# Kernel tuning notes

Measured on AMD Instinct MI355X. Metric: run time of the kernel, lower is better.

## Reference

```python
import jax, jax.numpy as jnp
import numpy as np

N = 100_000
E = 1_600_000
IN_FT, HID, OUT = 512, 128, 64


def setup_inputs() -> dict:
    key = jax.random.key(0)
    ks = jax.random.split(key, 7)
    x = jax.random.normal(ks[0], (N, IN_FT), dtype=jnp.float32)
    edge_index = jax.random.randint(ks[1], (2, E), 0, N, dtype=jnp.int32)
    edge_weight = jax.random.uniform(ks[2], (E,), dtype=jnp.float32)
    W1 = jax.random.normal(ks[3], (IN_FT, HID), dtype=jnp.float32) * 0.05
    b1 = jnp.zeros((HID,), dtype=jnp.float32)
    W2 = jax.random.normal(ks[4], (HID, OUT), dtype=jnp.float32) * 0.05
    b2 = jnp.zeros((OUT,), dtype=jnp.float32)
    return {"x": x, "edge_index": edge_index, "edge_weight": edge_weight,
            "W1": W1, "b1": b1, "W2": W2, "b2": b2}


def reference(x, edge_index, edge_weight, W1, b1, W2, b2):
    n = x.shape[0]
    row, col = edge_index[0], edge_index[1]
    # PyG gcn_norm: add self-loops with weight 1, symmetric normalization
    loop = jnp.arange(n, dtype=row.dtype)
    r = jnp.concatenate([row, loop])
    c = jnp.concatenate([col, loop])
    w = jnp.concatenate([edge_weight, jnp.ones((n,), edge_weight.dtype)])
    deg = jax.ops.segment_sum(w, c, num_segments=n)
    dinv = jnp.where(deg > 0, jax.lax.rsqrt(deg), 0.0)
    norm = dinv[r] * w * dinv[c]  # [E + N]

    def conv(h, W, b):
        h = h @ W                                  # [N, F_out]
        msg = norm[:, None] * h[r]                 # gather source nodes
        return jax.ops.segment_sum(msg, c, num_segments=n) + b

    h = jax.nn.relu(conv(x, W1, b1))
    # dropout: inference mode (training=False) -> identity
    out = conv(h, W2, b2)
    return jax.nn.log_softmax(out, axis=1)
```

## Files before the change

kernel.cpp:

```cpp
#include <hip/hip_runtime.h>
#include <hip/hip_fp16.h>


constexpr int NN  = 100000;
constexpr int NE  = 1600000;
constexpr int FIN = 512;
constexpr int FH  = 128;
constexpr int FO  = 64;
constexpr int CAP = 64;

constexpr int NBLK1 = 512;
constexpr int EPB   = NE / NBLK1;
constexpr int NBKT  = 196;
constexpr int BCAP  = 9728;

constexpr float WSCALE  = 32767.0f;
constexpr float IWSCALE = 1.0f / 32767.0f;

typedef _Float16 f16x8 __attribute__((ext_vector_type(8)));
typedef float    f32x4 __attribute__((ext_vector_type(4)));

union F16Frag { short4 s[2]; f16x8 v; };


__global__ __launch_bounds__(256) void k_prep(const float* __restrict__ W1,
                                              const float* __restrict__ W2,
                                              int* __restrict__ bcur,
                                              _Float16* __restrict__ w1t,
                                              _Float16* __restrict__ w2t) {
    int i = blockIdx.x * 256 + threadIdx.x;
    if (i < NBKT) bcur[i] = 0;
    if (i < FIN * FH) {
        int k = i >> 7, c = i & 127;
        w1t[c * FIN + k] = (_Float16)W1[i];
    } else if (i < FIN * FH + FH * FO) {
        int j = i - FIN * FH;
        int k = j >> 6, c = j & 63;
        w2t[c * FH + k] = (_Float16)W2[j];
    }
}


__global__ __launch_bounds__(256) void k_pass1(const int* __restrict__ rowi,
                                               const int* __restrict__ coli,
                                               const float* __restrict__ ew,
                                               int* __restrict__ bcur,
                                               unsigned long long* __restrict__ binned) {
    __shared__ unsigned long long buf[EPB];
    __shared__ int hist[NBKT];
    __shared__ int curs[NBKT];
    const int t = threadIdx.x;
    const int base = blockIdx.x * EPB;
    for (int i = t; i < NBKT; i += 256) hist[i] = 0;
    __syncthreads();
    for (int i = t; i < EPB; i += 256) {
        int e = base + i;
        int c = coli[e];
        unsigned wq = __float2uint_rn(ew[e] * WSCALE);
        buf[i] = ((unsigned long long)(unsigned)c << 32)
               | (unsigned long long)((wq << 17) | (unsigned)rowi[e]);
        atomicAdd(&hist[c >> 9], 1);
    }
    __syncthreads();
    if (t < NBKT) curs[t] = atomicAdd(&bcur[t], hist[t]);
    __syncthreads();
    for (int i = t; i < EPB; i += 256) {
        unsigned long long v = buf[i];
        int b = (int)(v >> 41);
        int pos = atomicAdd(&curs[b], 1);
        if ((unsigned)pos < BCAP) binned[(size_t)b * BCAP + pos] = v;
    }
}


__global__ __launch_bounds__(256) void k_pass2(const int* __restrict__ bcur,
                                               const unsigned long long* __restrict__ binned,
                                               unsigned* __restrict__ pay,
                                               int* __restrict__ cursor,
                                               float* __restrict__ dinv) {
    __shared__ int   cnt[512];
    __shared__ float wsum[512];
    const int t = threadIdx.x, b = blockIdx.x;
    for (int i = t; i < 512; i += 256) { cnt[i] = 0; wsum[i] = 0.f; }
    __syncthreads();
    const int total = min(bcur[b], BCAP);
    const int nbase = b * 512;
    for (int i = t; i < total; i += 256) {
        unsigned long long v = binned[(size_t)b * BCAP + i];
        int c9 = (int)((v >> 32) & 511);
        unsigned lo = (unsigned)v;
        int pos = atomicAdd(&cnt[c9], 1);
        atomicAdd(&wsum[c9], (float)(lo >> 17) * IWSCALE);
        if (pos < CAP) pay[(size_t)(nbase + c9) * CAP + pos] = lo;
    }
    __syncthreads();
    for (int i = t; i < 512; i += 256) {
        int node = nbase + i;
        if (node < NN) {
            cursor[node] = cnt[i];
            dinv[node]   = rsqrtf(1.0f + wsum[i]);
        }
    }
}


__global__ __launch_bounds__(256) void k_gemm1(const float* __restrict__ X,
                                               const _Float16* __restrict__ w1t,
                                               _Float16* __restrict__ H1) {
    __shared__ __align__(16) _Float16 As[128 * 64];
    __shared__ __align__(16) _Float16 Bs[128 * 64];
    const int tid  = threadIdx.x;
    const int brow = blockIdx.x * 128;
    const int wid = tid >> 6, l = tid & 63;
    const int wr = wid >> 1, wc = wid & 1;
    const int l15 = l & 15, lg = l >> 4;

    f32x4 acc[4][4];
#pragma unroll
    for (int m = 0; m < 4; ++m)
#pragma unroll
        for (int n = 0; n < 4; ++n) acc[m][n] = (f32x4){0.f, 0.f, 0.f, 0.f};

    const int ar  = tid >> 1;
    const int as0 = (tid & 1) * 4;
    const int grow = brow + ar;

    for (int k0 = 0; k0 < FIN; k0 += 64) {
#pragma unroll
        for (int i = 0; i < 4; ++i) {
            int slot = as0 + i;
            float4 lo = make_float4(0.f, 0.f, 0.f, 0.f), hi = lo;
            if (grow < NN) {
                lo = *(const float4*)&X[(size_t)grow * FIN + k0 + slot * 8];
                hi = *(const float4*)&X[(size_t)grow * FIN + k0 + slot * 8 + 4];
            }
            union { _Float16 h[8]; int4 v; } pk;
            pk.h[0] = (_Float16)lo.x; pk.h[1] = (_Float16)lo.y;
            pk.h[2] = (_Float16)lo.z; pk.h[3] = (_Float16)lo.w;
            pk.h[4] = (_Float16)hi.x; pk.h[5] = (_Float16)hi.y;
            pk.h[6] = (_Float16)hi.z; pk.h[7] = (_Float16)hi.w;
            *(int4*)&As[ar * 64 + ((slot ^ (ar & 7)) * 8)] = pk.v;
        }
#pragma unroll
        for (int i = 0; i < 4; ++i) {
            int slot = as0 + i;
            *(int4*)&Bs[ar * 64 + ((slot ^ (ar & 7)) * 8)] =
                *(const int4*)&w1t[ar * FIN + k0 + slot * 8];
        }
        __syncthreads();
#pragma unroll
        for (int ks = 0; ks < 2; ++ks) {
            F16Frag au[4], bu[4];
            int klo = ks * 32 + 4 * lg;
            int khi = klo + 16;
#pragma unroll
            for (int m = 0; m < 4; ++m) {
                int row = wr * 64 + m * 16 + l15;
                int sw  = row & 7;
                au[m].s[0] = *(const short4*)&As[row * 64 + (((klo >> 3) ^ sw) * 8) + (klo & 7)];
                au[m].s[1] = *(const short4*)&As[row * 64 + (((khi >> 3) ^ sw) * 8) + (khi & 7)];
            }
#pragma unroll
            for (int n = 0; n < 4; ++n) {
                int row = wc * 64 + n * 16 + l15;
                int sw  = row & 7;
                bu[n].s[0] = *(const short4*)&Bs[row * 64 + (((klo >> 3) ^ sw) * 8) + (klo & 7)];
                bu[n].s[1] = *(const short4*)&Bs[row * 64 + (((khi >> 3) ^ sw) * 8) + (khi & 7)];
            }
#pragma unroll
            for (int m = 0; m < 4; ++m)
#pragma unroll
                for (int n = 0; n < 4; ++n)
                    acc[m][n] = __builtin_amdgcn_mfma_f32_16x16x32_f16(
                        au[m].v, bu[n].v, acc[m][n], 0, 0, 0);
        }
        __syncthreads();
    }
#pragma unroll
    for (int m = 0; m < 4; ++m)
#pragma unroll
        for (int n = 0; n < 4; ++n) {
            int gcol = wc * 64 + n * 16 + l15;
#pragma unroll
            for (int r = 0; r < 4; ++r) {
                int gr = brow + wr * 64 + m * 16 + lg * 4 + r;
                if (gr < NN) H1[(size_t)gr * FH + gcol] = (_Float16)acc[m][n][r];
            }
        }
}


__global__ __launch_bounds__(256) void k_gemm2(const _Float16* __restrict__ H2,
                                               const _Float16* __restrict__ w2t,
                                               _Float16* __restrict__ H3) {
    __shared__ __align__(16) _Float16 As[128 * 128];
    __shared__ __align__(16) _Float16 Bs[64 * 128];
    const int tid  = threadIdx.x;
    const int brow = blockIdx.x * 128;
    const int wid = tid >> 6, l = tid & 63;
    const int wr = wid >> 1, wc = wid & 1;
    const int l15 = l & 15, lg = l >> 4;

    f32x4 acc[4][2];
#pragma unroll
    for (int m = 0; m < 4; ++m)
#pragma unroll
        for (int n = 0; n < 2; ++n) acc[m][n] = (f32x4){0.f, 0.f, 0.f, 0.f};

    {
        int ar = tid >> 1, grow = brow + ar;
#pragma unroll
        for (int i = 0; i < 8; ++i) {
            int slot = (tid & 1) * 8 + i;
            int4 v = make_int4(0, 0, 0, 0);
            if (grow < NN) v = *(const int4*)&H2[(size_t)grow * FH + slot * 8];
            *(int4*)&As[ar * 128 + ((slot ^ (ar & 15)) * 8)] = v;
        }
        int br = tid >> 2;
#pragma unroll
        for (int i = 0; i < 4; ++i) {
            int slot = (tid & 3) * 4 + i;
            *(int4*)&Bs[br * 128 + ((slot ^ (br & 15)) * 8)] =
                *(const int4*)&w2t[br * FH + slot * 8];
        }
    }
    __syncthreads();
#pragma unroll
    for (int ks = 0; ks < 4; ++ks) {
        F16Frag au[4], bu[2];
        int klo = ks * 32 + 4 * lg;
        int khi = klo + 16;
#pragma unroll
        for (int m = 0; m < 4; ++m) {
            int row = wr * 64 + m * 16 + l15;
            int sw  = row & 15;
            au[m].s[0] = *(const short4*)&As[row * 128 + (((klo >> 3) ^ sw) * 8) + (klo & 7)];
            au[m].s[1] = *(const short4*)&As[row * 128 + (((khi >> 3) ^ sw) * 8) + (khi & 7)];
        }
#pragma unroll
        for (int n = 0; n < 2; ++n) {
            int row = wc * 32 + n * 16 + l15;
            int sw  = row & 15;
            bu[n].s[0] = *(const short4*)&Bs[row * 128 + (((klo >> 3) ^ sw) * 8) + (klo & 7)];
            bu[n].s[1] = *(const short4*)&Bs[row * 128 + (((khi >> 3) ^ sw) * 8) + (khi & 7)];
        }
#pragma unroll
        for (int m = 0; m < 4; ++m)
#pragma unroll
            for (int n = 0; n < 2; ++n)
                acc[m][n] = __builtin_amdgcn_mfma_f32_16x16x32_f16(
                    au[m].v, bu[n].v, acc[m][n], 0, 0, 0);
    }
#pragma unroll
    for (int m = 0; m < 4; ++m)
#pragma unroll
        for (int n = 0; n < 2; ++n) {
            int gcol = wc * 32 + n * 16 + l15;
#pragma unroll
            for (int r = 0; r < 4; ++r) {
                int gr = brow + wr * 64 + m * 16 + lg * 4 + r;
                if (gr < NN) H3[(size_t)gr * FO + gcol] = (_Float16)acc[m][n][r];
            }
        }
}


__global__ __launch_bounds__(256) void k_agg1(const int* __restrict__ cursor,
                                              const unsigned* __restrict__ pay,
                                              const float* __restrict__ dinv,
                                              const __half* __restrict__ H1,
                                              const float* __restrict__ b1,
                                              __half* __restrict__ H2) {
    int node = (blockIdx.x * 256 + threadIdx.x) >> 6;
    int lane = threadIdx.x & 63;
    if (node >= NN) return;
    const int f = lane * 2;
    float dc = dinv[node];
    float2 hc = __half22float2(*(const __half2*)&H1[(size_t)node * FH + f]);
    float a0x = dc * dc * hc.x, a0y = dc * dc * hc.y;
    float a1x = 0, a1y = 0, a2x = 0, a2y = 0, a3x = 0, a3y = 0;
    int cnt = min(max(cursor[node], 0), CAP);
    const unsigned* p = &pay[(size_t)node * CAP];
    int e = 0;
    for (; e + 4 <= cnt; e += 4) {
        unsigned v0 = p[e], v1 = p[e + 1], v2 = p[e + 2], v3 = p[e + 3];
        int s0 = v0 & 0x1FFFF, s1 = v1 & 0x1FFFF;
        int s2 = v2 & 0x1FFFF, s3 = v3 & 0x1FFFF;
        float w0 = (float)(v0 >> 17) * IWSCALE * dinv[s0] * dc;
        float w1 = (float)(v1 >> 17) * IWSCALE * dinv[s1] * dc;
        float w2 = (float)(v2 >> 17) * IWSCALE * dinv[s2] * dc;
        float w3 = (float)(v3 >> 17) * IWSCALE * dinv[s3] * dc;
        float2 g0 = __half22float2(*(const __half2*)&H1[(size_t)s0 * FH + f]);
        float2 g1 = __half22float2(*(const __half2*)&H1[(size_t)s1 * FH + f]);
        float2 g2 = __half22float2(*(const __half2*)&H1[(size_t)s2 * FH + f]);
        float2 g3 = __half22float2(*(const __half2*)&H1[(size_t)s3 * FH + f]);
        a0x += w0 * g0.x; a0y += w0 * g0.y;
        a1x += w1 * g1.x; a1y += w1 * g1.y;
        a2x += w2 * g2.x; a2y += w2 * g2.y;
        a3x += w3 * g3.x; a3y += w3 * g3.y;
    }
    for (; e < cnt; ++e) {
        unsigned v = p[e];
        int s = v & 0x1FFFF;
        float w = (float)(v >> 17) * IWSCALE * dinv[s] * dc;
        float2 g = __half22float2(*(const __half2*)&H1[(size_t)s * FH + f]);
        a0x += w * g.x; a0y += w * g.y;
    }
    float vx = a0x + a1x + a2x + a3x + b1[f];
    float vy = a0y + a1y + a2y + a3y + b1[f + 1];
    vx = vx > 0.f ? vx : 0.f;
    vy = vy > 0.f ? vy : 0.f;
    *(__half2*)&H2[(size_t)node * FH + f] = __floats2half2_rn(vx, vy);
}


__global__ __launch_bounds__(256) void k_agg2(const int* __restrict__ cursor,
                                              const unsigned* __restrict__ pay,
                                              const float* __restrict__ dinv,
                                              const __half* __restrict__ H3,
                                              const float* __restrict__ b2,
                                              float* __restrict__ out) {
    int node = (blockIdx.x * 256 + threadIdx.x) >> 6;
    int lane = threadIdx.x & 63;
    if (node >= NN) return;
    float dc = dinv[node];
    float a0 = dc * dc * __half2float(H3[(size_t)node * FO + lane]);
    float a1 = 0, a2 = 0, a3 = 0;
    int cnt = min(max(cursor[node], 0), CAP);
    const unsigned* p = &pay[(size_t)node * CAP];
    int e = 0;
    for (; e + 4 <= cnt; e += 4) {
        unsigned v0 = p[e], v1 = p[e + 1], v2 = p[e + 2], v3 = p[e + 3];
        int s0 = v0 & 0x1FFFF, s1 = v1 & 0x1FFFF;
        int s2 = v2 & 0x1FFFF, s3 = v3 & 0x1FFFF;
        float w0 = (float)(v0 >> 17) * IWSCALE * dinv[s0] * dc;
        float w1 = (float)(v1 >> 17) * IWSCALE * dinv[s1] * dc;
        float w2 = (float)(v2 >> 17) * IWSCALE * dinv[s2] * dc;
        float w3 = (float)(v3 >> 17) * IWSCALE * dinv[s3] * dc;
        a0 += w0 * __half2float(H3[(size_t)s0 * FO + lane]);
        a1 += w1 * __half2float(H3[(size_t)s1 * FO + lane]);
        a2 += w2 * __half2float(H3[(size_t)s2 * FO + lane]);
        a3 += w3 * __half2float(H3[(size_t)s3 * FO + lane]);
    }
    for (; e < cnt; ++e) {
        unsigned v = p[e];
        int s = v & 0x1FFFF;
        float w = (float)(v >> 17) * IWSCALE * dinv[s] * dc;
        a0 += w * __half2float(H3[(size_t)s * FO + lane]);
    }
    float v = a0 + a1 + a2 + a3 + b2[lane];
    float m = v;
#pragma unroll
    for (int s = 32; s; s >>= 1) m = fmaxf(m, __shfl_xor(m, s));
    float ex = expf(v - m);
    float sum = ex;
#pragma unroll
    for (int s = 32; s; s >>= 1) sum += __shfl_xor(sum, s);
    out[(size_t)node * FO + lane] = v - m - logf(sum);
}


extern "C" void kernel_launch(void* const* d_in, const int* in_sizes, int n_in,
                              void* d_out, int out_size, void* d_ws, size_t ws_size,
                              hipStream_t stream) {
    const float* x   = (const float*)d_in[0];
    const int*   ei  = (const int*)d_in[1];
    const int*   row = ei;
    const int*   col = ei + NE;
    const float* ew  = (const float*)d_in[2];
    const float* W1  = (const float*)d_in[3];
    const float* b1  = (const float*)d_in[4];
    const float* W2  = (const float*)d_in[5];
    const float* b2  = (const float*)d_in[6];
    float* out = (float*)d_out;

    int*       bcur   = (int*)d_ws;
    int*       cursor = bcur + 256;
    float*     dinv   = (float*)(cursor + 102400);
    _Float16*  w1t    = (_Float16*)(dinv + 102400);
    _Float16*  w2t    = w1t + FIN * FH;
    unsigned long long* binned = (unsigned long long*)(w2t + FH * FO);
    unsigned*  pay    = (unsigned*)(binned + (size_t)NBKT * BCAP);
    _Float16*  H1     = (_Float16*)(pay + (size_t)NN * CAP);
    _Float16*  H2     = H1 + (size_t)NN * FH;
    _Float16*  H3     = H2 + (size_t)NN * FH;

    k_prep <<<(FIN * FH + FH * FO + 255) / 256, 256, 0, stream>>>(W1, W2, bcur, w1t, w2t);
    k_pass1<<<NBLK1, 256, 0, stream>>>(row, col, ew, bcur, binned);
    k_pass2<<<NBKT, 256, 0, stream>>>(bcur, binned, pay, cursor, dinv);

    k_gemm1<<<(NN + 127) / 128, 256, 0, stream>>>(x, w1t, H1);
    k_agg1 <<<(NN * 64 + 255) / 256, 256, 0, stream>>>(cursor, pay, dinv,
                                                       (const __half*)H1, b1, (__half*)H2);
    k_gemm2<<<(NN + 127) / 128, 256, 0, stream>>>(H2, w2t, H3);
    k_agg2 <<<(NN * 64 + 255) / 256, 256, 0, stream>>>(cursor, pay, dinv,
                                                       (const __half*)H3, b2, out);
}
```

Measured before the change: 287.4 us.

## Halve GEMM row tiles and register-prefetch next K-slice in gemm1

Both GEMM kernels now use 64-row tiles instead of 128, which doubles the grid size and raises occupancy through launch_bounds(256,4). In gemm1, the next 64-wide K slice of X and W1 is loaded into registers while the current slice is staged into shared memory and multiplied, so global-load latency overlaps with MFMA work. The aim is to hide the cost of streaming X, the 200MB fp32 input that dominates. The trade-off is more blocks that each reload the W tile, and less MFMA reuse per block.

```diff
diff --git a/kernel.cpp b/kernel.cpp
--- a/kernel.cpp
+++ b/kernel.cpp
@@ -104,58 +104,74 @@
 }
 
 
-__global__ __launch_bounds__(256) void k_gemm1(const float* __restrict__ X,
-                                               const _Float16* __restrict__ w1t,
-                                               _Float16* __restrict__ H1) {
-    __shared__ __align__(16) _Float16 As[128 * 64];
+__global__ __launch_bounds__(256, 4) void k_gemm1(const float* __restrict__ X,
+                                                  const _Float16* __restrict__ w1t,
+                                                  _Float16* __restrict__ H1) {
+    __shared__ __align__(16) _Float16 As[64 * 64];
     __shared__ __align__(16) _Float16 Bs[128 * 64];
     const int tid  = threadIdx.x;
-    const int brow = blockIdx.x * 128;
+    const int brow = blockIdx.x * 64;
     const int wid = tid >> 6, l = tid & 63;
     const int wr = wid >> 1, wc = wid & 1;
     const int l15 = l & 15, lg = l >> 4;
 
-    f32x4 acc[4][4];
-#pragma unroll
-    for (int m = 0; m < 4; ++m)
+    f32x4 acc[2][4];
+#pragma unroll
+    for (int m = 0; m < 2; ++m)
 #pragma unroll
         for (int n = 0; n < 4; ++n) acc[m][n] = (f32x4){0.f, 0.f, 0.f, 0.f};
 
-    const int ar  = tid >> 1;
-    const int as0 = (tid & 1) * 4;
+    const int ar   = tid >> 2;
+    const int apart= tid & 3;
     const int grow = brow + ar;
+    const int br   = tid >> 1;
+    const int bhalf= tid & 1;
+
+    float4 xa[4];
+    int4   wb[4];
+
+#pragma unroll
+    for (int j = 0; j < 4; ++j) {
+        xa[j] = (grow < NN) ? *(const float4*)&X[(size_t)grow * FIN + apart * 16 + j * 4]
+                            : make_float4(0.f, 0.f, 0.f, 0.f);
+        wb[j] = *(const int4*)&w1t[br * FIN + bhalf * 32 + j * 8];
+    }
 
     for (int k0 = 0; k0 < FIN; k0 += 64) {
 #pragma unroll
-        for (int i = 0; i < 4; ++i) {
-            int slot = as0 + i;
-            float4 lo = make_float4(0.f, 0.f, 0.f, 0.f), hi = lo;
-            if (grow < NN) {
-                lo = *(const float4*)&X[(size_t)grow * FIN + k0 + slot * 8];
-                hi = *(const float4*)&X[(size_t)grow * FIN + k0 + slot * 8 + 4];
+        for (int h = 0; h < 2; ++h) {
+            union { _Float16 f[8]; int4 v; } pk;
+            float4 a = xa[h * 2], b = xa[h * 2 + 1];
+            pk.f[0] = (_Float16)a.x; pk.f[1] = (_Float16)a.y;
+            pk.f[2] = (_Float16)a.z; pk.f[3] = (_Float16)a.w;
+            pk.f[4] = (_Float16)b.x; pk.f[5] = (_Float16)b.y;
+            pk.f[6] = (_Float16)b.z; pk.f[7] = (_Float16)b.w;
+            int slot = apart * 2 + h;
+            *(int4*)&As[ar * 64 + ((slot ^ (ar & 7)) * 8)] = pk.v;
+        }
+#pragma unroll
+        for (int j = 0; j < 4; ++j) {
+            int slot = bhalf * 4 + j;
+            *(int4*)&Bs[br * 64 + ((slot ^ (br & 7)) * 8)] = wb[j];
+        }
+        if (k0 + 64 < FIN) {
+#pragma unroll
+            for (int j = 0; j < 4; ++j) {
+                xa[j] = (grow < NN)
+                    ? *(const float4*)&X[(size_t)grow * FIN + k0 + 64 + apart * 16 + j * 4]
+                    : make_float4(0.f, 0.f, 0.f, 0.f);
+                wb[j] = *(const int4*)&w1t[br * FIN + k0 + 64 + bhalf * 32 + j * 8];
             }
-            union { _Float16 h[8]; int4 v; } pk;
-            pk.h[0] = (_Float16)lo.x; pk.h[1] = (_Float16)lo.y;
-            pk.h[2] = (_Float16)lo.z; pk.h[3] = (_Float16)lo.w;
-            pk.h[4] = (_Float16)hi.x; pk.h[5] = (_Float16)hi.y;
-            pk.h[6] = (_Float16)hi.z; pk.h[7] = (_Float16)hi.w;
-            *(int4*)&As[ar * 64 + ((slot ^ (ar & 7)) * 8)] = pk.v;
-        }
-#pragma unroll
-        for (int i = 0; i < 4; ++i) {
-            int slot = as0 + i;
-            *(int4*)&Bs[ar * 64 + ((slot ^ (ar & 7)) * 8)] =
-                *(const int4*)&w1t[ar * FIN + k0 + slot * 8];
         }
         __syncthreads();
 #pragma unroll
         for (int ks = 0; ks < 2; ++ks) {
-            F16Frag au[4], bu[4];
+            F16Frag au[2], bu[4];
             int klo = ks * 32 + 4 * lg;
             int khi = klo + 16;
 #pragma unroll
-            for (int m = 0; m < 4; ++m) {
-                int row = wr * 64 + m * 16 + l15;
+            for (int m = 0; m < 2; ++m) {
+                int row = wr * 32 + m * 16 + l15;
                 int sw  = row & 7;
                 au[m].s[0] = *(const short4*)&As[row * 64 + (((klo >> 3) ^ sw) * 8) + (klo & 7)];
                 au[m].s[1] = *(const short4*)&As[row * 64 + (((khi >> 3) ^ sw) * 8) + (khi & 7)];
@@ -168,7 +184,7 @@
                 bu[n].s[1] = *(const short4*)&Bs[row * 64 + (((khi >> 3) ^ sw) * 8) + (khi & 7)];
             }
 #pragma unroll
-            for (int m = 0; m < 4; ++m)
+            for (int m = 0; m < 2; ++m)
 #pragma unroll
                 for (int n = 0; n < 4; ++n)
                     acc[m][n] = __builtin_amdgcn_mfma_f32_16x16x32_f16(
@@ -177,62 +193,57 @@
         __syncthreads();
     }
 #pragma unroll
-    for (int m = 0; m < 4; ++m)
+    for (int m = 0; m < 2; ++m)
 #pragma unroll
         for (int n = 0; n < 4; ++n) {
             int gcol = wc * 64 + n * 16 + l15;
 #pragma unroll
             for (int r = 0; r < 4; ++r) {
-                int gr = brow + wr * 64 + m * 16 + lg * 4 + r;
+                int gr = brow + wr * 32 + m * 16 + lg * 4 + r;
                 if (gr < NN) H1[(size_t)gr * FH + gcol] = (_Float16)acc[m][n][r];
             }
         }
 }
 
 
-__global__ __launch_bounds__(256) void k_gemm2(const _Float16* __restrict__ H2,
-                                               const _Float16* __restrict__ w2t,
-                                               _Float16* __restrict__ H3) {
-    __shared__ __align__(16) _Float16 As[128 * 128];
+__global__ __launch_bounds__(256, 4) void k_gemm2(const _Float16* __restrict__ H2,
+                                                  const _Float16* __restrict__ w2t,
+                                                  _Float16* __restrict__ H3) {
+    __shared__ __align__(16) _Float16 As[64 * 128];
     __shared__ __align__(16) _Float16 Bs[64 * 128];
     const int tid  = threadIdx.x;
-    const int brow = blockIdx.x * 128;
+    const int brow = blockIdx.x * 64;
     const int wid = tid >> 6, l = tid & 63;
     const int wr = wid >> 1, wc = wid & 1;
     const int l15 = l & 15, lg = l >> 4;
 
-    f32x4 acc[4][2];
-#pragma unroll
-    for (int m = 0; m < 4; ++m)
+    f32x4 acc[2][2];
+#pragma unroll
+    for (int m = 0; m < 2; ++m)
 #pragma unroll
         for (int n = 0; n < 2; ++n) acc[m][n] = (f32x4){0.f, 0.f, 0.f, 0.f};
 
     {
-        int ar = tid >> 1, grow = brow + ar;
-#pragma unroll
-        for (int i = 0; i < 8; ++i) {
-            int slot = (tid & 1) * 8 + i;
+        int ar = tid >> 2, part = tid & 3, grow = brow + ar;
+#pragma unroll
+        for (int j = 0; j < 4; ++j) {
+            int slot = part * 4 + j;
             int4 v = make_int4(0, 0, 0, 0);
             if (grow < NN) v = *(const int4*)&H2[(size_t)grow * FH + slot * 8];
             *(int4*)&As[ar * 128 + ((slot ^ (ar & 15)) * 8)] = v;
-        }
-        int br = tid >> 2;
-#pragma unroll
-        for (int i = 0; i < 4; ++i) {
-            int slot = (tid & 3) * 4 + i;
-            *(int4*)&Bs[br * 128 + ((slot ^ (br & 15)) * 8)] =
-                *(const int4*)&w2t[br * FH + slot * 8];
+            *(int4*)&Bs[ar * 128 + ((slot ^ (ar & 15)) * 8)] =
+                *(const int4*)&w2t[ar * FH + slot * 8];
         }
     }
     __syncthreads();
 #pragma unroll
     for (int ks = 0; ks < 4; ++ks) {
-        F16Frag au[4], bu[2];
+        F16Frag au[2], bu[2];
         int klo = ks * 32 + 4 * lg;
         int khi = klo + 16;
 #pragma unroll
-        for (int m = 0; m < 4; ++m) {
-            int row = wr * 64 + m * 16 + l15;
+        for (int m = 0; m < 2; ++m) {
+            int row = wr * 32 + m * 16 + l15;
             int sw  = row & 15;
             au[m].s[0] = *(const short4*)&As[row * 128 + (((klo >> 3) ^ sw) * 8) + (klo & 7)];
             au[m].s[1] = *(const short4*)&As[row * 128 + (((khi >> 3) ^ sw) * 8) + (khi & 7)];
@@ -245,20 +256,20 @@
             bu[n].s[1] = *(const short4*)&Bs[row * 128 + (((khi >> 3) ^ sw) * 8) + (khi & 7)];
         }
 #pragma unroll
-        for (int m = 0; m < 4; ++m)
+        for (int m = 0; m < 2; ++m)
 #pragma unroll
             for (int n = 0; n < 2; ++n)
                 acc[m][n] = __builtin_amdgcn_mfma_f32_16x16x32_f16(
                     au[m].v, bu[n].v, acc[m][n], 0, 0, 0);
     }
 #pragma unroll
-    for (int m = 0; m < 4; ++m)
+    for (int m = 0; m < 2; ++m)
 #pragma unroll
         for (int n = 0; n < 2; ++n) {
             int gcol = wc * 32 + n * 16 + l15;
 #pragma unroll
             for (int r = 0; r < 4; ++r) {
-                int gr = brow + wr * 64 + m * 16 + lg * 4 + r;
+                int gr = brow + wr * 32 + m * 16 + lg * 4 + r;
                 if (gr < NN) H3[(size_t)gr * FO + gcol] = (_Float16)acc[m][n][r];
             }
         }
@@ -389,10 +400,10 @@
     k_pass1<<<NBLK1, 256, 0, stream>>>(row, col, ew, bcur, binned);
     k_pass2<<<NBKT, 256, 0, stream>>>(bcur, binned, pay, cursor, dinv);
 
-    k_gemm1<<<(NN + 127) / 128, 256, 0, stream>>>(x, w1t, H1);
+    k_gemm1<<<(NN + 63) / 64, 256, 0, stream>>>(x, w1t, H1);
     k_agg1 <<<(NN * 64 + 255) / 256, 256, 0, stream>>>(cursor, pay, dinv,
                                                        (const __half*)H1, b1, (__half*)H2);
-    k_gemm2<<<(NN + 127) / 128, 256, 0, stream>>>(H2, w2t, H3);
+    k_gemm2<<<(NN + 63) / 64, 256, 0, stream>>>(H2, w2t, H3);
     k_agg2 <<<(NN * 64 + 255) / 256, 256, 0, stream>>>(cursor, pay, dinv,
                                                        (const __half*)H3, b2, out);
 }
```

Result: slower. 353.6 us (+23.0%).
